# Performance work log

Measured on AMD Instinct MI355X. Metric: run time of the kernel, lower is better.

## Reference

```python
import jax, jax.numpy as jnp
import numpy as np

W_WORDS, T_TOKENS, N_EMBD, N_HIDDEN = 4096, 32768, 512, 2048
MASK_DENSITY = 0.004  # ~ avg word covers a handful of char positions


def setup_inputs() -> dict:
    key = jax.random.key(0)
    k1, k2, k3, k4, k5 = jax.random.split(key, 5)
    in_words = jax.random.normal(k1, (W_WORDS, N_EMBD), dtype=jnp.float32)
    x = jax.random.normal(k2, (T_TOKENS, N_EMBD), dtype=jnp.float32)
    attention_mask = jax.random.bernoulli(k3, MASK_DENSITY, (W_WORDS, T_TOKENS))
    W_fc = jax.random.normal(k4, (N_EMBD, N_HIDDEN), dtype=jnp.float32) * (1.0 / np.sqrt(N_EMBD))
    W_proj = jax.random.normal(k5, (N_HIDDEN, N_EMBD), dtype=jnp.float32) * (1.0 / np.sqrt(N_HIDDEN))
    return {"in_words": in_words, "x": x, "attention_mask": attention_mask,
            "W_fc": W_fc, "W_proj": W_proj}


def reference(in_words, x, attention_mask, W_fc, W_proj):
    # MLP with residual (dropout = identity at eval): words [W, D]
    h = jax.nn.gelu(in_words @ W_fc, approximate=False)  # [W, H], exact GELU like nn.GELU()
    words = h @ W_proj + in_words                         # [W, D]
    # Per-word masked scatter-add into x_new. The sequential python loop
    # x_new[mask_i] += words[i] is additive across i, so it equals
    # x + mask^T @ words (mask promoted to float for the contraction).
    x_new = x + jnp.einsum('wt,wd->td', attention_mask.astype(words.dtype), words)
    return words, x_new
```

## Files before the change

kernel.cpp:

```cpp
#include <hip/hip_runtime.h>
#include <hip/hip_bf16.h>
#include <math.h>

#define W_WORDS  4096
#define T_TOKENS 32768
#define N_EMBD   512
#define N_HIDDEN 2048
#define CAP      64

typedef __attribute__((ext_vector_type(8))) short bf16x8;
typedef __attribute__((ext_vector_type(4))) float f32x4;
typedef __attribute__((ext_vector_type(4))) int   i32x4;
typedef unsigned int u32;

#define GLOBAL_AS __attribute__((address_space(1)))
#define LDS_AS    __attribute__((address_space(3)))

__global__ __launch_bounds__(256) void scan_prep_kernel(
    const int* __restrict__ mask, int* __restrict__ counts,
    unsigned short* __restrict__ lists,
    const float* __restrict__ in_words, __hip_bfloat16* __restrict__ words_bf,
    const float* __restrict__ W_fc,     __hip_bfloat16* __restrict__ WfcT,
    const float* __restrict__ W_proj,   __hip_bfloat16* __restrict__ WprojT)
{
    __shared__ float tile[32][33];
    const int b = blockIdx.x;

    if (b < 32768) {
        const size_t base = (size_t)b * 4096 + (size_t)threadIdx.x * 4;
        i32x4 v[4];
#pragma unroll
        for (int k = 0; k < 4; ++k)
            v[k] = __builtin_nontemporal_load((const i32x4*)(mask + base + (size_t)k * 1024));
#pragma unroll
        for (int k = 0; k < 4; ++k) {
            if ((v[k].x | v[k].y | v[k].z | v[k].w) == 0) continue;
            const size_t e = base + (size_t)k * 1024;
            const int w  = (int)(e >> 15);
            const int t0 = (int)(e & (T_TOKENS - 1));
            if (v[k].x) { const int p = atomicAdd(&counts[t0+0], 1); if (p < CAP) lists[(size_t)(t0+0)*CAP+p] = (unsigned short)w; }
            if (v[k].y) { const int p = atomicAdd(&counts[t0+1], 1); if (p < CAP) lists[(size_t)(t0+1)*CAP+p] = (unsigned short)w; }
            if (v[k].z) { const int p = atomicAdd(&counts[t0+2], 1); if (p < CAP) lists[(size_t)(t0+2)*CAP+p] = (unsigned short)w; }
            if (v[k].w) { const int p = atomicAdd(&counts[t0+3], 1); if (p < CAP) lists[(size_t)(t0+3)*CAP+p] = (unsigned short)w; }
        }
        return;
    }

    const int p = b - 32768;
    if (p < 1024) {
        const size_t gid = (size_t)p * 256 + threadIdx.x;
        const float4 a0 = ((const float4*)in_words)[2 * gid];
        const float4 a1 = ((const float4*)in_words)[2 * gid + 1];
        union { __hip_bfloat16 t[8]; bf16x8 v; } u;
        u.t[0] = __float2bfloat16(a0.x); u.t[1] = __float2bfloat16(a0.y);
        u.t[2] = __float2bfloat16(a0.z); u.t[3] = __float2bfloat16(a0.w);
        u.t[4] = __float2bfloat16(a1.x); u.t[5] = __float2bfloat16(a1.y);
        u.t[6] = __float2bfloat16(a1.z); u.t[7] = __float2bfloat16(a1.w);
        *(bf16x8*)(words_bf + 8 * gid) = u.v;
        return;
    }
    {
        const float* in;  __hip_bfloat16* out; int R, C, bx, by;
        if (p < 2048) { in = W_fc;   out = WfcT;   R = N_EMBD;   C = N_HIDDEN;
                        const int l = p - 1024; bx = l & 63; by = l >> 6; }
        else          { in = W_proj; out = WprojT; R = N_HIDDEN; C = N_EMBD;
                        const int l = p - 2048; bx = l & 15; by = l >> 4; }
        const int tx = threadIdx.x & 31, ty = threadIdx.x >> 5;
        const int r0 = by * 32, c0 = bx * 32;
#pragma unroll
        for (int i = 0; i < 4; ++i) {
            const int r = ty + i * 8;
            tile[r][tx] = in[(size_t)(r0 + r) * C + c0 + tx];
        }
        __syncthreads();
#pragma unroll
        for (int i = 0; i < 4; ++i) {
            const int r = ty + i * 8;
            out[(size_t)(c0 + r) * R + r0 + tx] = __float2bfloat16(tile[tx][r]);
        }
    }
}

template <int BM, int BN, int MODE, int KSUB, int GRIDN, int NTILES>
__global__ __launch_bounds__(512) void gemm_bf16_mfma_kernel(
    const __hip_bfloat16* __restrict__ A,
    const __hip_bfloat16* __restrict__ BT,
    const float* __restrict__ Res,
    void* __restrict__ Cout,
    __hip_bfloat16* __restrict__ Cbf,
    int M, int N, int K)
{
    constexpr int NTHR   = 512;
    constexpr int WVN    = 4;
    constexpr int WM     = BM / 2, WN = BN / WVN;
    constexpr int FM     = WM / 16, FN = WN / 16;
    constexpr int BK     = 32 * KSUB;
    constexpr int TILE_B = (BM + BN) * 64;
    constexpr int NISS   = TILE_B / (NTHR * 16);
    constexpr int BUFSZ  = TILE_B * KSUB;

    __shared__ __align__(16) char smem[2 * BUFSZ];

    const int tid  = (int)threadIdx.x;
    const int lane = tid & 63;
    const int wid  = tid >> 6;
    const int wm   = wid >> 2, wn = wid & 3;

    const int bid = (int)blockIdx.x;
    const int g   = (bid & 7) * (NTILES / 8) + (bid >> 3);
    const int bm  = (g / GRIDN) * BM;
    const int bn  = (g % GRIDN) * BN;

    auto stage = [&](char* dst, int k0) {
#pragma unroll
        for (int ks = 0; ks < KSUB; ++ks) {
            const int kk = k0 + ks * 32;
#pragma unroll
            for (int is = 0; is < NISS; ++is) {
                const int boff = (is * NTHR + tid) * 16;
                const __hip_bfloat16* src;
                if (boff < BM * 64) {
                    const int row = boff >> 6, kb = boff & 63;
                    src = A + (size_t)(bm + row) * K + kk + (kb >> 1);
                } else {
                    const int bo = boff - BM * 64;
                    const int row = bo >> 6, kb = bo & 63;
                    src = BT + (size_t)(bn + row) * K + kk + (kb >> 1);
                }
                __builtin_amdgcn_global_load_lds(
                    (const GLOBAL_AS u32*)(const void*)src,
                    (LDS_AS u32*)(void*)(dst + ks * TILE_B + boff), 16, 0, 0);
            }
        }
    };

    f32x4 acc[FM][FN] = {};

    stage(smem, 0);
    __syncthreads();

    const int nt = K / BK;
    int cur = 0;
    for (int t = 0; t < nt; ++t) {
        if (t + 1 < nt) stage(smem + (cur ^ 1) * BUFSZ, (t + 1) * BK);

        char* buf = smem + cur * BUFSZ;
#pragma unroll
        for (int ks = 0; ks < KSUB; ++ks) {
            char* As = buf + ks * TILE_B;
            char* Bs = As + BM * 64;
            bf16x8 af[FM], bfq[FN];
#pragma unroll
            for (int i = 0; i < FM; ++i) {
                const int row = wm * WM + i * 16 + (lane & 15);
                af[i] = *(const bf16x8*)(As + row * 64 + (lane >> 4) * 16);
            }
#pragma unroll
            for (int j = 0; j < FN; ++j) {
                const int col = wn * WN + j * 16 + (lane & 15);
                bfq[j] = *(const bf16x8*)(Bs + col * 64 + (lane >> 4) * 16);
            }
#pragma unroll
            for (int i = 0; i < FM; ++i)
#pragma unroll
                for (int j = 0; j < FN; ++j)
                    acc[i][j] = __builtin_amdgcn_mfma_f32_16x16x32_bf16(
                        af[i], bfq[j], acc[i][j], 0, 0, 0);
        }
        __syncthreads();
        cur ^= 1;
    }

#pragma unroll
    for (int i = 0; i < FM; ++i) {
        const int row0 = bm + wm * WM + i * 16 + (lane >> 4) * 4;
#pragma unroll
        for (int j = 0; j < FN; ++j) {
            const int col = bn + wn * WN + j * 16 + (lane & 15);
#pragma unroll
            for (int r = 0; r < 4; ++r) {
                const int row = row0 + r;
                float v = acc[i][j][r];
                if (MODE == 0) {
                    v = 0.5f * v * (1.0f + erff(v * 0.70710678118654752440f));
                    ((__hip_bfloat16*)Cout)[(size_t)row * N + col] = __float2bfloat16(v);
                } else {
                    const float vv = v + Res[(size_t)row * N + col];
                    ((float*)Cout)[(size_t)row * N + col] = vv;
                    Cbf[(size_t)row * N + col] = __float2bfloat16(vv);
                }
            }
        }
    }
}

__device__ inline void acc_bf8(f32x4& a, f32x4& b, bf16x8 r)
{
    a.x += __uint_as_float(((u32)(unsigned short)r[0]) << 16);
    a.y += __uint_as_float(((u32)(unsigned short)r[1]) << 16);
    a.z += __uint_as_float(((u32)(unsigned short)r[2]) << 16);
    a.w += __uint_as_float(((u32)(unsigned short)r[3]) << 16);
    b.x += __uint_as_float(((u32)(unsigned short)r[4]) << 16);
    b.y += __uint_as_float(((u32)(unsigned short)r[5]) << 16);
    b.z += __uint_as_float(((u32)(unsigned short)r[6]) << 16);
    b.w += __uint_as_float(((u32)(unsigned short)r[7]) << 16);
}

__global__ __launch_bounds__(256) void scatter_add_kernel(
    const float* __restrict__ x, const __hip_bfloat16* __restrict__ words_bf,
    const int* __restrict__ counts, const unsigned short* __restrict__ lists,
    float* __restrict__ x_new)
{
    const int t = __builtin_amdgcn_readfirstlane(
        (int)blockIdx.x * 4 + ((int)threadIdx.x >> 6));
    const int lane = threadIdx.x & 63;
    const size_t base = (size_t)t * N_EMBD + lane * 8;

    f32x4 c0a = __builtin_nontemporal_load((const f32x4*)(x + base));
    f32x4 c0b = __builtin_nontemporal_load((const f32x4*)(x + base + 4));
    f32x4 c1a = {0.f,0.f,0.f,0.f}, c1b = {0.f,0.f,0.f,0.f};
    f32x4 c2a = {0.f,0.f,0.f,0.f}, c2b = {0.f,0.f,0.f,0.f};
    f32x4 c3a = {0.f,0.f,0.f,0.f}, c3b = {0.f,0.f,0.f,0.f};

    const int cnt = min(counts[t], CAP);
    const unsigned short* lst = &lists[(size_t)t * CAP];

    int i = 0;
    for (; i + 4 <= cnt; i += 4) {
        const bf16x8 r0 = *(const bf16x8*)(words_bf + (size_t)lst[i]     * N_EMBD + lane * 8);
        const bf16x8 r1 = *(const bf16x8*)(words_bf + (size_t)lst[i + 1] * N_EMBD + lane * 8);
        const bf16x8 r2 = *(const bf16x8*)(words_bf + (size_t)lst[i + 2] * N_EMBD + lane * 8);
        const bf16x8 r3 = *(const bf16x8*)(words_bf + (size_t)lst[i + 3] * N_EMBD + lane * 8);
        acc_bf8(c0a, c0b, r0);
        acc_bf8(c1a, c1b, r1);
        acc_bf8(c2a, c2b, r2);
        acc_bf8(c3a, c3b, r3);
    }
    for (; i < cnt; ++i) {
        const bf16x8 r0 = *(const bf16x8*)(words_bf + (size_t)lst[i] * N_EMBD + lane * 8);
        acc_bf8(c0a, c0b, r0);
    }
    c0a += c1a; c2a += c3a; c0a += c2a;
    c0b += c1b; c2b += c3b; c0b += c2b;
    __builtin_nontemporal_store(c0a, (f32x4*)(x_new + base));
    __builtin_nontemporal_store(c0b, (f32x4*)(x_new + base + 4));
}

extern "C" void kernel_launch(void* const* d_in, const int* in_sizes, int n_in,
                              void* d_out, int out_size, void* d_ws, size_t ws_size,
                              hipStream_t stream)
{
    const float* in_words = (const float*)d_in[0];
    const float* x        = (const float*)d_in[1];
    const int*   mask     = (const int*)d_in[2];
    const float* W_fc     = (const float*)d_in[3];
    const float* W_proj   = (const float*)d_in[4];

    float* out_words = (float*)d_out;
    float* out_x     = out_words + (size_t)W_WORDS * N_EMBD;

    char* ws = (char*)d_ws;
    __hip_bfloat16* words_bf = (__hip_bfloat16*)(ws);
    __hip_bfloat16* WfcT     = (__hip_bfloat16*)(ws + (4u << 20));
    __hip_bfloat16* WprojT   = (__hip_bfloat16*)(ws + (6u << 20));
    __hip_bfloat16* h_bf     = (__hip_bfloat16*)(ws + (8u << 20));
    __hip_bfloat16* wout_bf  = (__hip_bfloat16*)(ws + (24u << 20));
    int*            counts   = (int*)(ws + (28u << 20));
    unsigned short* lists    = (unsigned short*)(ws + (28u << 20) + T_TOKENS * 4);

    hipMemsetAsync(counts, 0, (size_t)T_TOKENS * sizeof(int), stream);

    scan_prep_kernel<<<35840, 256, 0, stream>>>(
        mask, counts, lists, in_words, words_bf, W_fc, WfcT, W_proj, WprojT);

    gemm_bf16_mfma_kernel<128, 128, 0, 2, 16, 512>
        <<<512, 512, 0, stream>>>(
            words_bf, WfcT, nullptr, h_bf, nullptr, W_WORDS, N_HIDDEN, N_EMBD);

    gemm_bf16_mfma_kernel<64, 64, 1, 4, 8, 512>
        <<<512, 512, 0, stream>>>(
            h_bf, WprojT, in_words, out_words, wout_bf, W_WORDS, N_EMBD, N_HIDDEN);

    scatter_add_kernel<<<T_TOKENS / 4, 256, 0, stream>>>(
        x, wout_bf, counts, lists, out_x);
}
```

Before: 197.5 us.

## Fuse mask scan into scatter-add with LDS accumulation per token tile

Drops the atomic-based per-token list building, the counts memset and the separate scatter kernel. A new kernel gives each block 32 tokens and copies their x rows into 64KB of LDS. It then walks all 4096 word rows of the mask, using wave ballots to find nonzeros and adding the matching bf16 word rows into the LDS accumulators. This removes the atomics and list traffic, but the mask is now read in narrow strided column slices. The large LDS footprint also limits occupancy, which could expose memory latency.

```diff
diff --git a/kernel.cpp b/kernel.cpp
--- a/kernel.cpp
+++ b/kernel.cpp
@@ -6,19 +6,15 @@
 #define T_TOKENS 32768
 #define N_EMBD   512
 #define N_HIDDEN 2048
-#define CAP      64
 
 typedef __attribute__((ext_vector_type(8))) short bf16x8;
 typedef __attribute__((ext_vector_type(4))) float f32x4;
-typedef __attribute__((ext_vector_type(4))) int   i32x4;
 typedef unsigned int u32;
 
 #define GLOBAL_AS __attribute__((address_space(1)))
 #define LDS_AS    __attribute__((address_space(3)))
 
-__global__ __launch_bounds__(256) void scan_prep_kernel(
-    const int* __restrict__ mask, int* __restrict__ counts,
-    unsigned short* __restrict__ lists,
+__global__ __launch_bounds__(256) void prep_kernel(
     const float* __restrict__ in_words, __hip_bfloat16* __restrict__ words_bf,
     const float* __restrict__ W_fc,     __hip_bfloat16* __restrict__ WfcT,
     const float* __restrict__ W_proj,   __hip_bfloat16* __restrict__ WprojT)
@@ -26,29 +22,8 @@
     __shared__ float tile[32][33];
     const int b = blockIdx.x;
 
-    if (b < 32768) {
-        const size_t base = (size_t)b * 4096 + (size_t)threadIdx.x * 4;
-        i32x4 v[4];
-#pragma unroll
-        for (int k = 0; k < 4; ++k)
-            v[k] = __builtin_nontemporal_load((const i32x4*)(mask + base + (size_t)k * 1024));
-#pragma unroll
-        for (int k = 0; k < 4; ++k) {
-            if ((v[k].x | v[k].y | v[k].z | v[k].w) == 0) continue;
-            const size_t e = base + (size_t)k * 1024;
-            const int w  = (int)(e >> 15);
-            const int t0 = (int)(e & (T_TOKENS - 1));
-            if (v[k].x) { const int p = atomicAdd(&counts[t0+0], 1); if (p < CAP) lists[(size_t)(t0+0)*CAP+p] = (unsigned short)w; }
-            if (v[k].y) { const int p = atomicAdd(&counts[t0+1], 1); if (p < CAP) lists[(size_t)(t0+1)*CAP+p] = (unsigned short)w; }
-            if (v[k].z) { const int p = atomicAdd(&counts[t0+2], 1); if (p < CAP) lists[(size_t)(t0+2)*CAP+p] = (unsigned short)w; }
-            if (v[k].w) { const int p = atomicAdd(&counts[t0+3], 1); if (p < CAP) lists[(size_t)(t0+3)*CAP+p] = (unsigned short)w; }
-        }
-        return;
-    }
-
-    const int p = b - 32768;
-    if (p < 1024) {
-        const size_t gid = (size_t)p * 256 + threadIdx.x;
+    if (b < 1024) {
+        const size_t gid = (size_t)b * 256 + threadIdx.x;
         const float4 a0 = ((const float4*)in_words)[2 * gid];
         const float4 a1 = ((const float4*)in_words)[2 * gid + 1];
         union { __hip_bfloat16 t[8]; bf16x8 v; } u;
@@ -61,10 +36,10 @@
     }
     {
         const float* in;  __hip_bfloat16* out; int R, C, bx, by;
-        if (p < 2048) { in = W_fc;   out = WfcT;   R = N_EMBD;   C = N_HIDDEN;
-                        const int l = p - 1024; bx = l & 63; by = l >> 6; }
+        if (b < 2048) { in = W_fc;   out = WfcT;   R = N_EMBD;   C = N_HIDDEN;
+                        const int l = b - 1024; bx = l & 63; by = l >> 6; }
         else          { in = W_proj; out = WprojT; R = N_HIDDEN; C = N_EMBD;
-                        const int l = p - 2048; bx = l & 15; by = l >> 4; }
+                        const int l = b - 2048; bx = l & 15; by = l >> 4; }
         const int tx = threadIdx.x & 31, ty = threadIdx.x >> 5;
         const int r0 = by * 32, c0 = bx * 32;
 #pragma unroll
@@ -194,56 +169,70 @@
     }
 }
 
-__device__ inline void acc_bf8(f32x4& a, f32x4& b, bf16x8 r)
-{
-    a.x += __uint_as_float(((u32)(unsigned short)r[0]) << 16);
-    a.y += __uint_as_float(((u32)(unsigned short)r[1]) << 16);
-    a.z += __uint_as_float(((u32)(unsigned short)r[2]) << 16);
-    a.w += __uint_as_float(((u32)(unsigned short)r[3]) << 16);
-    b.x += __uint_as_float(((u32)(unsigned short)r[4]) << 16);
-    b.y += __uint_as_float(((u32)(unsigned short)r[5]) << 16);
-    b.z += __uint_as_float(((u32)(unsigned short)r[6]) << 16);
-    b.w += __uint_as_float(((u32)(unsigned short)r[7]) << 16);
-}
-
-__global__ __launch_bounds__(256) void scatter_add_kernel(
-    const float* __restrict__ x, const __hip_bfloat16* __restrict__ words_bf,
-    const int* __restrict__ counts, const unsigned short* __restrict__ lists,
+__device__ inline float bf2f(short s)
+{
+    return __uint_as_float(((u32)(unsigned short)s) << 16);
+}
+
+__global__ __launch_bounds__(256) void scan_scatter_kernel(
+    const int* __restrict__ mask,
+    const float* __restrict__ x,
+    const __hip_bfloat16* __restrict__ wout_bf,
     float* __restrict__ x_new)
 {
-    const int t = __builtin_amdgcn_readfirstlane(
-        (int)blockIdx.x * 4 + ((int)threadIdx.x >> 6));
-    const int lane = threadIdx.x & 63;
-    const size_t base = (size_t)t * N_EMBD + lane * 8;
-
-    f32x4 c0a = __builtin_nontemporal_load((const f32x4*)(x + base));
-    f32x4 c0b = __builtin_nontemporal_load((const f32x4*)(x + base + 4));
-    f32x4 c1a = {0.f,0.f,0.f,0.f}, c1b = {0.f,0.f,0.f,0.f};
-    f32x4 c2a = {0.f,0.f,0.f,0.f}, c2b = {0.f,0.f,0.f,0.f};
-    f32x4 c3a = {0.f,0.f,0.f,0.f}, c3b = {0.f,0.f,0.f,0.f};
-
-    const int cnt = min(counts[t], CAP);
-    const unsigned short* lst = &lists[(size_t)t * CAP];
-
-    int i = 0;
-    for (; i + 4 <= cnt; i += 4) {
-        const bf16x8 r0 = *(const bf16x8*)(words_bf + (size_t)lst[i]     * N_EMBD + lane * 8);
-        const bf16x8 r1 = *(const bf16x8*)(words_bf + (size_t)lst[i + 1] * N_EMBD + lane * 8);
-        const bf16x8 r2 = *(const bf16x8*)(words_bf + (size_t)lst[i + 2] * N_EMBD + lane * 8);
-        const bf16x8 r3 = *(const bf16x8*)(words_bf + (size_t)lst[i + 3] * N_EMBD + lane * 8);
-        acc_bf8(c0a, c0b, r0);
-        acc_bf8(c1a, c1b, r1);
-        acc_bf8(c2a, c2b, r2);
-        acc_bf8(c3a, c3b, r3);
-    }
-    for (; i < cnt; ++i) {
-        const bf16x8 r0 = *(const bf16x8*)(words_bf + (size_t)lst[i] * N_EMBD + lane * 8);
-        acc_bf8(c0a, c0b, r0);
-    }
-    c0a += c1a; c2a += c3a; c0a += c2a;
-    c0b += c1b; c2b += c3b; c0b += c2b;
-    __builtin_nontemporal_store(c0a, (f32x4*)(x_new + base));
-    __builtin_nontemporal_store(c0b, (f32x4*)(x_new + base + 4));
+    extern __shared__ float acc[];
+    const int t0   = (int)blockIdx.x * 32;
+    const int tid  = (int)threadIdx.x;
+    const int lane = tid & 63;
+    const int wv   = tid >> 6;
+
+    {
+        const f32x4* src = (const f32x4*)(x + (size_t)t0 * N_EMBD);
+        f32x4* dst = (f32x4*)acc;
+        for (int j = tid; j < (32 * N_EMBD) / 4; j += 256)
+            dst[j] = src[j];
+    }
+    __syncthreads();
+
+    const int tok   = t0 + wv * 8 + (lane & 7);
+    const int tbase = wv * 8;
+
+    for (int i = 0; i < 64; ++i) {
+        int v[8];
+#pragma unroll
+        for (int u = 0; u < 8; ++u) {
+            const int w = i * 64 + u * 8 + (lane >> 3);
+            v[u] = __builtin_nontemporal_load(mask + (size_t)w * T_TOKENS + tok);
+        }
+#pragma unroll
+        for (int u = 0; u < 8; ++u) {
+            unsigned long long m = __ballot(v[u] != 0);
+            while (m) {
+                const int b = (int)__ffsll((unsigned long long)m) - 1;
+                m &= (m - 1);
+                const int w  = i * 64 + u * 8 + (b >> 3);
+                const int tl = tbase + (b & 7);
+                const bf16x8 r = *(const bf16x8*)(wout_bf + (size_t)w * N_EMBD + lane * 8);
+                float* arow = acc + tl * N_EMBD + lane * 8;
+                f32x4 a0 = *(const f32x4*)(arow);
+                f32x4 a1 = *(const f32x4*)(arow + 4);
+                a0.x += bf2f(r[0]); a0.y += bf2f(r[1]);
+                a0.z += bf2f(r[2]); a0.w += bf2f(r[3]);
+                a1.x += bf2f(r[4]); a1.y += bf2f(r[5]);
+                a1.z += bf2f(r[6]); a1.w += bf2f(r[7]);
+                *(f32x4*)(arow)     = a0;
+                *(f32x4*)(arow + 4) = a1;
+            }
+        }
+    }
+    __syncthreads();
+
+    {
+        f32x4* dst = (f32x4*)(x_new + (size_t)t0 * N_EMBD);
+        const f32x4* src = (const f32x4*)acc;
+        for (int j = tid; j < (32 * N_EMBD) / 4; j += 256)
+            __builtin_nontemporal_store(src[j], dst + j);
+    }
 }
 
 extern "C" void kernel_launch(void* const* d_in, const int* in_sizes, int n_in,
@@ -265,13 +254,9 @@
     __hip_bfloat16* WprojT   = (__hip_bfloat16*)(ws + (6u << 20));
     __hip_bfloat16* h_bf     = (__hip_bfloat16*)(ws + (8u << 20));
     __hip_bfloat16* wout_bf  = (__hip_bfloat16*)(ws + (24u << 20));
-    int*            counts   = (int*)(ws + (28u << 20));
-    unsigned short* lists    = (unsigned short*)(ws + (28u << 20) + T_TOKENS * 4);
-
-    hipMemsetAsync(counts, 0, (size_t)T_TOKENS * sizeof(int), stream);
-
-    scan_prep_kernel<<<35840, 256, 0, stream>>>(
-        mask, counts, lists, in_words, words_bf, W_fc, WfcT, W_proj, WprojT);
+
+    prep_kernel<<<3072, 256, 0, stream>>>(in_words, words_bf, W_fc, WfcT,
+                                          W_proj, WprojT);
 
     gemm_bf16_mfma_kernel<128, 128, 0, 2, 16, 512>
         <<<512, 512, 0, stream>>>(
@@ -281,6 +266,6 @@
         <<<512, 512, 0, stream>>>(
             h_bf, WprojT, in_words, out_words, wout_bf, W_WORDS, N_EMBD, N_HIDDEN);
 
-    scatter_add_kernel<<<T_TOKENS / 4, 256, 0, stream>>>(
-        x, wout_bf, counts, lists, out_x);
-}
+    scan_scatter_kernel<<<T_TOKENS / 32, 256, 32 * N_EMBD * sizeof(float), stream>>>(
+        mask, x, wout_bf, out_x);
+}
```

After: 410.5 us. 108% more time.
